# Kernel tuning notes

Hardware: AMD Instinct MI355X
Metric: run time of the kernel (lower is better)

Reference implementation:

```python
import jax, jax.numpy as jnp
import numpy as np

NUM_LABELS = 1024
NUM_CAMS = 8


def setup_inputs() -> dict:
    key = jax.random.key(0)
    k1, k2, k3 = jax.random.split(key, 3)
    feats = jax.random.normal(k1, (16384, 2048), dtype=jnp.float32)
    labels = jax.random.randint(k2, (16384,), 0, NUM_LABELS, dtype=jnp.int64)
    cam_ids = jax.random.randint(k3, (16384,), 0, NUM_CAMS, dtype=jnp.int64)
    return {"feats": feats, "labels": labels, "cam_ids": cam_ids}


def reference(feats, labels, cam_ids):
    # Combined (person-id, camera-id) segment id -> fused segment-mean.
    seg = labels * NUM_CAMS + cam_ids  # [N]
    num_segments = NUM_LABELS * NUM_CAMS
    sums = jax.ops.segment_sum(feats, seg, num_segments=num_segments)  # [S, D]
    counts = jax.ops.segment_sum(jnp.ones_like(seg, dtype=feats.dtype), seg,
                                 num_segments=num_segments)  # [S]
    means = sums / jnp.maximum(counts, 1.0)[:, None]
    # targets[i] = mean of feats over group(label_i, cam_i); detached in torch.
    targets = jax.lax.stop_gradient(means[seg])  # [N, D]
    # SmoothL1 (beta=1), reduction='mean'
    d = feats - targets
    ad = jnp.abs(d)
    loss = jnp.mean(jnp.where(ad < 1.0, 0.5 * d * d, ad - 0.5))
    return loss
```

## Files before the change

### kernel.cpp

```cpp
#include <hip/hip_runtime.h>
#include <hip/hip_bf16.h>

#define N_ROWS 16384
#define D_COLS 2048
#define NUM_LABELS 1024
#define NUM_CAMS 8
#define NUM_SEG (NUM_LABELS * NUM_CAMS)
#define MAXPER 64

__global__ void build_lists_kernel(const int* __restrict__ labels,
                                   const int* __restrict__ cams,
                                   int* __restrict__ counts,
                                   int* __restrict__ lists) {
    int i = blockIdx.x * blockDim.x + threadIdx.x;
    if (i < N_ROWS) {
        int seg = labels[i] * NUM_CAMS + cams[i];
        int pos = atomicAdd(&counts[seg], 1);
        if (pos < MAXPER) lists[seg * MAXPER + pos] = i;
    }
}

__device__ __forceinline__ float smooth_l1(float d) {
    float ad = fabsf(d);
    return ad < 1.0f ? 0.5f * d * d : ad - 0.5f;
}

__global__ __launch_bounds__(256) void seg_loss_kernel(const float* __restrict__ feats,
                                                       const int* __restrict__ counts,
                                                       const int* __restrict__ lists,
                                                       float* __restrict__ partials) {
    int seg = blockIdx.x;
    int tid = threadIdx.x;
    int cnt = counts[seg];
    float local = 0.0f;

    __shared__ int slist[MAXPER];

    if (cnt > 0) {
        int rows = cnt < MAXPER ? cnt : MAXPER;

        if (tid < rows) slist[tid] = lists[seg * MAXPER + tid];
        __syncthreads();

        float m0x = 0.f, m0y = 0.f, m0z = 0.f, m0w = 0.f;
        float m1x = 0.f, m1y = 0.f, m1z = 0.f, m1w = 0.f;

        for (int r = 0; r < rows; ++r) {
            const float4* rp = (const float4*)(feats + (size_t)slist[r] * D_COLS);
            float4 a = rp[tid];
            float4 b = rp[tid + 256];
            m0x += a.x; m0y += a.y; m0z += a.z; m0w += a.w;
            m1x += b.x; m1y += b.y; m1z += b.z; m1w += b.w;
        }
        float inv = 1.0f / (float)cnt;
        m0x *= inv; m0y *= inv; m0z *= inv; m0w *= inv;
        m1x *= inv; m1y *= inv; m1z *= inv; m1w *= inv;

        for (int r = 0; r < rows; ++r) {
            const float4* rp = (const float4*)(feats + (size_t)slist[r] * D_COLS);
            float4 a = rp[tid];
            float4 b = rp[tid + 256];
            local += smooth_l1(a.x - m0x) + smooth_l1(a.y - m0y)
                   + smooth_l1(a.z - m0z) + smooth_l1(a.w - m0w);
            local += smooth_l1(b.x - m1x) + smooth_l1(b.y - m1y)
                   + smooth_l1(b.z - m1z) + smooth_l1(b.w - m1w);
        }
    }

    for (int o = 32; o > 0; o >>= 1)
        local += __shfl_down(local, o, 64);

    __shared__ float wsum[4];
    int lane = tid & 63;
    int wid  = tid >> 6;
    if (lane == 0) wsum[wid] = local;
    __syncthreads();
    if (tid == 0)
        partials[seg] = wsum[0] + wsum[1] + wsum[2] + wsum[3];
}

__global__ __launch_bounds__(256) void reduce_kernel(const float* __restrict__ partials,
                                                     float* __restrict__ out) {
    int tid = threadIdx.x;
    float s = 0.0f;
    for (int i = tid; i < NUM_SEG; i += 256)
        s += partials[i];

    for (int o = 32; o > 0; o >>= 1)
        s += __shfl_down(s, o, 64);

    __shared__ float wsum[4];
    int lane = tid & 63;
    int wid  = tid >> 6;
    if (lane == 0) wsum[wid] = s;
    __syncthreads();
    if (tid == 0)
        out[0] = (wsum[0] + wsum[1] + wsum[2] + wsum[3])
               * (1.0f / ((float)N_ROWS * (float)D_COLS));
}

extern "C" void kernel_launch(void* const* d_in, const int* in_sizes, int n_in,
                              void* d_out, int out_size, void* d_ws, size_t ws_size,
                              hipStream_t stream) {
    const float* feats = (const float*)d_in[0];
    const int* labels  = (const int*)d_in[1];
    const int* cams    = (const int*)d_in[2];
    float* out = (float*)d_out;

    int* counts     = (int*)d_ws;
    int* lists      = counts + NUM_SEG;
    float* partials = (float*)(lists + NUM_SEG * MAXPER);

    hipMemsetAsync(counts, 0, NUM_SEG * sizeof(int), stream);

    build_lists_kernel<<<(N_ROWS + 255) / 256, 256, 0, stream>>>(labels, cams, counts, lists);
    seg_loss_kernel<<<NUM_SEG, 256, 0, stream>>>(feats, counts, lists, partials);
    reduce_kernel<<<1, 256, 0, stream>>>(partials, out);
}
```

Baseline: 213.6 us.

## Assign each half-segment to one wavefront, drop shared memory and block syncs

Reworks the segment loss kernel so each 64-lane wavefront handles half the columns of one segment, with 4 float4 loads per row per lane instead of 2. Row indices are held in lane registers and broadcast with __shfl, which removes the shared-memory list and __syncthreads barriers. Each wave writes its own partial, so the final reduce now covers twice as many partials. The intent is finer-grained scheduling and more loads in flight per thread, at the cost of more accumulator registers and the row-index load being repeated by both waves of a segment.

Result: slower. 219.0 us (+2.6%).

```diff
diff --git a/kernel.cpp b/kernel.cpp
--- a/kernel.cpp
+++ b/kernel.cpp
@@ -7,6 +7,8 @@
 #define NUM_CAMS 8
 #define NUM_SEG (NUM_LABELS * NUM_CAMS)
 #define MAXPER 64
+#define F4_PER_ROW (D_COLS / 4)
+#define NUM_WAVES (NUM_SEG * 2)
 
 __global__ void build_lists_kernel(const int* __restrict__ labels,
                                    const int* __restrict__ cams,
@@ -29,61 +31,73 @@
                                                        const int* __restrict__ counts,
                                                        const int* __restrict__ lists,
                                                        float* __restrict__ partials) {
-    int seg = blockIdx.x;
-    int tid = threadIdx.x;
-    int cnt = counts[seg];
-    float local = 0.0f;
-
-    __shared__ int slist[MAXPER];
+    int wave = (blockIdx.x * 256 + threadIdx.x) >> 6;
+    int lane = threadIdx.x & 63;
+    int seg  = wave >> 1;
+    int half = wave & 1;
+    int cnt  = counts[seg];
+    float loss = 0.0f;
 
     if (cnt > 0) {
         int rows = cnt < MAXPER ? cnt : MAXPER;
 
-        if (tid < rows) slist[tid] = lists[seg * MAXPER + tid];
-        __syncthreads();
+        int myidx = (lane < rows) ? lists[seg * MAXPER + lane] : 0;
 
-        float m0x = 0.f, m0y = 0.f, m0z = 0.f, m0w = 0.f;
-        float m1x = 0.f, m1y = 0.f, m1z = 0.f, m1w = 0.f;
+        const float4* base = (const float4*)feats;
+        int coff = half * 256 + lane;
+
+        float s0x=0.f,s0y=0.f,s0z=0.f,s0w=0.f;
+        float s1x=0.f,s1y=0.f,s1z=0.f,s1w=0.f;
+        float s2x=0.f,s2y=0.f,s2z=0.f,s2w=0.f;
+        float s3x=0.f,s3y=0.f,s3z=0.f,s3w=0.f;
 
         for (int r = 0; r < rows; ++r) {
-            const float4* rp = (const float4*)(feats + (size_t)slist[r] * D_COLS);
-            float4 a = rp[tid];
-            float4 b = rp[tid + 256];
-            m0x += a.x; m0y += a.y; m0z += a.z; m0w += a.w;
-            m1x += b.x; m1y += b.y; m1z += b.z; m1w += b.w;
+            int row = __shfl(myidx, r, 64);
+            const float4* rp = base + (size_t)row * F4_PER_ROW + coff;
+            float4 t0 = rp[0];
+            float4 t1 = rp[64];
+            float4 t2 = rp[128];
+            float4 t3 = rp[192];
+            s0x += t0.x; s0y += t0.y; s0z += t0.z; s0w += t0.w;
+            s1x += t1.x; s1y += t1.y; s1z += t1.z; s1w += t1.w;
+            s2x += t2.x; s2y += t2.y; s2z += t2.z; s2w += t2.w;
+            s3x += t3.x; s3y += t3.y; s3z += t3.z; s3w += t3.w;
         }
         float inv = 1.0f / (float)cnt;
-        m0x *= inv; m0y *= inv; m0z *= inv; m0w *= inv;
-        m1x *= inv; m1y *= inv; m1z *= inv; m1w *= inv;
+        s0x*=inv; s0y*=inv; s0z*=inv; s0w*=inv;
+        s1x*=inv; s1y*=inv; s1z*=inv; s1w*=inv;
+        s2x*=inv; s2y*=inv; s2z*=inv; s2w*=inv;
+        s3x*=inv; s3y*=inv; s3z*=inv; s3w*=inv;
 
         for (int r = 0; r < rows; ++r) {
-            const float4* rp = (const float4*)(feats + (size_t)slist[r] * D_COLS);
-            float4 a = rp[tid];
-            float4 b = rp[tid + 256];
-            local += smooth_l1(a.x - m0x) + smooth_l1(a.y - m0y)
-                   + smooth_l1(a.z - m0z) + smooth_l1(a.w - m0w);
-            local += smooth_l1(b.x - m1x) + smooth_l1(b.y - m1y)
-                   + smooth_l1(b.z - m1z) + smooth_l1(b.w - m1w);
+            int row = __shfl(myidx, r, 64);
+            const float4* rp = base + (size_t)row * F4_PER_ROW + coff;
+            float4 t0 = rp[0];
+            float4 t1 = rp[64];
+            float4 t2 = rp[128];
+            float4 t3 = rp[192];
+            loss += smooth_l1(t0.x - s0x) + smooth_l1(t0.y - s0y)
+                  + smooth_l1(t0.z - s0z) + smooth_l1(t0.w - s0w);
+            loss += smooth_l1(t1.x - s1x) + smooth_l1(t1.y - s1y)
+                  + smooth_l1(t1.z - s1z) + smooth_l1(t1.w - s1w);
+            loss += smooth_l1(t2.x - s2x) + smooth_l1(t2.y - s2y)
+                  + smooth_l1(t2.z - s2z) + smooth_l1(t2.w - s2w);
+            loss += smooth_l1(t3.x - s3x) + smooth_l1(t3.y - s3y)
+                  + smooth_l1(t3.z - s3z) + smooth_l1(t3.w - s3w);
         }
     }
 
     for (int o = 32; o > 0; o >>= 1)
-        local += __shfl_down(local, o, 64);
-
-    __shared__ float wsum[4];
-    int lane = tid & 63;
-    int wid  = tid >> 6;
-    if (lane == 0) wsum[wid] = local;
-    __syncthreads();
-    if (tid == 0)
-        partials[seg] = wsum[0] + wsum[1] + wsum[2] + wsum[3];
+        loss += __shfl_down(loss, o, 64);
+    if (lane == 0)
+        partials[wave] = loss;
 }
 
 __global__ __launch_bounds__(256) void reduce_kernel(const float* __restrict__ partials,
                                                      float* __restrict__ out) {
     int tid = threadIdx.x;
     float s = 0.0f;
-    for (int i = tid; i < NUM_SEG; i += 256)
+    for (int i = tid; i < NUM_WAVES; i += 256)
         s += partials[i];
 
     for (int o = 32; o > 0; o >>= 1)
@@ -114,6 +128,6 @@
     hipMemsetAsync(counts, 0, NUM_SEG * sizeof(int), stream);
 
     build_lists_kernel<<<(N_ROWS + 255) / 256, 256, 0, stream>>>(labels, cams, counts, lists);
-    seg_loss_kernel<<<NUM_SEG, 256, 0, stream>>>(feats, counts, lists, partials);
+    seg_loss_kernel<<<NUM_WAVES * 64 / 256, 256, 0, stream>>>(feats, counts, lists, partials);
     reduce_kernel<<<1, 256, 0, stream>>>(partials, out);
 }
```

## Cache segment rows in registers and split each segment across two blocks

Applied to the files above, without the earlier changes.

Each segment is now handled by two blocks, each covering half of the columns, which doubles the grid and gives each thread one float4 per row instead of two. Up to 12 rows per segment are loaded once into registers and reused for both the mean pass and the loss pass, which removes the second global read for typical segment sizes (about 2 rows on average). Loads are issued unconditionally, using masked list indices and zero weights, so they can all be in flight at once. The cost is extra loads for unused slots (stale list entries, masked into range) and higher register pressure.

New measurement: 224.3 us. 1.05x slower.

```diff
diff --git a/kernel.cpp b/kernel.cpp
--- a/kernel.cpp
+++ b/kernel.cpp
@@ -7,6 +7,9 @@
 #define NUM_CAMS 8
 #define NUM_SEG (NUM_LABELS * NUM_CAMS)
 #define MAXPER 64
+#define R_REG 12
+#define F4_PER_ROW (D_COLS / 4)
+#define NUM_BLOCKS (NUM_SEG * 2)
 
 __global__ void build_lists_kernel(const int* __restrict__ labels,
                                    const int* __restrict__ cams,
@@ -29,61 +32,76 @@
                                                        const int* __restrict__ counts,
                                                        const int* __restrict__ lists,
                                                        float* __restrict__ partials) {
-    int seg = blockIdx.x;
-    int tid = threadIdx.x;
+    int bid  = blockIdx.x;
+    int seg  = bid >> 1;
+    int half = bid & 1;
+    int tid  = threadIdx.x;
+
+    __shared__ int slist[R_REG];
+
+    if (tid < R_REG)
+        slist[tid] = lists[seg * MAXPER + tid] & (N_ROWS - 1);
     int cnt = counts[seg];
-    float local = 0.0f;
+    __syncthreads();
 
-    __shared__ int slist[MAXPER];
+    int rows = cnt < MAXPER ? cnt : MAXPER;
 
-    if (cnt > 0) {
-        int rows = cnt < MAXPER ? cnt : MAXPER;
+    const float4* base = (const float4*)feats + (half * 256 + tid);
 
-        if (tid < rows) slist[tid] = lists[seg * MAXPER + tid];
-        __syncthreads();
+    float4 v[R_REG];
+#pragma unroll
+    for (int r = 0; r < R_REG; ++r)
+        v[r] = base[(size_t)slist[r] * F4_PER_ROW];
 
-        float m0x = 0.f, m0y = 0.f, m0z = 0.f, m0w = 0.f;
-        float m1x = 0.f, m1y = 0.f, m1z = 0.f, m1w = 0.f;
+    float mx = 0.f, my = 0.f, mz = 0.f, mw = 0.f;
+#pragma unroll
+    for (int r = 0; r < R_REG; ++r) {
+        float w = (r < rows) ? 1.0f : 0.0f;
+        mx = fmaf(w, v[r].x, mx);
+        my = fmaf(w, v[r].y, my);
+        mz = fmaf(w, v[r].z, mz);
+        mw = fmaf(w, v[r].w, mw);
+    }
+    for (int r = R_REG; r < rows; ++r) {
+        int row = lists[seg * MAXPER + r];
+        float4 a = base[(size_t)row * F4_PER_ROW];
+        mx += a.x; my += a.y; mz += a.z; mw += a.w;
+    }
 
-        for (int r = 0; r < rows; ++r) {
-            const float4* rp = (const float4*)(feats + (size_t)slist[r] * D_COLS);
-            float4 a = rp[tid];
-            float4 b = rp[tid + 256];
-            m0x += a.x; m0y += a.y; m0z += a.z; m0w += a.w;
-            m1x += b.x; m1y += b.y; m1z += b.z; m1w += b.w;
-        }
-        float inv = 1.0f / (float)cnt;
-        m0x *= inv; m0y *= inv; m0z *= inv; m0w *= inv;
-        m1x *= inv; m1y *= inv; m1z *= inv; m1w *= inv;
+    float inv = 1.0f / (float)(cnt > 0 ? cnt : 1);
+    mx *= inv; my *= inv; mz *= inv; mw *= inv;
 
-        for (int r = 0; r < rows; ++r) {
-            const float4* rp = (const float4*)(feats + (size_t)slist[r] * D_COLS);
-            float4 a = rp[tid];
-            float4 b = rp[tid + 256];
-            local += smooth_l1(a.x - m0x) + smooth_l1(a.y - m0y)
-                   + smooth_l1(a.z - m0z) + smooth_l1(a.w - m0w);
-            local += smooth_l1(b.x - m1x) + smooth_l1(b.y - m1y)
-                   + smooth_l1(b.z - m1z) + smooth_l1(b.w - m1w);
-        }
+    float loss = 0.0f;
+#pragma unroll
+    for (int r = 0; r < R_REG; ++r) {
+        float w = (r < rows) ? 1.0f : 0.0f;
+        loss += w * (smooth_l1(v[r].x - mx) + smooth_l1(v[r].y - my)
+                   + smooth_l1(v[r].z - mz) + smooth_l1(v[r].w - mw));
+    }
+    for (int r = R_REG; r < rows; ++r) {
+        int row = lists[seg * MAXPER + r];
+        float4 a = base[(size_t)row * F4_PER_ROW];
+        loss += smooth_l1(a.x - mx) + smooth_l1(a.y - my)
+              + smooth_l1(a.z - mz) + smooth_l1(a.w - mw);
     }
 
     for (int o = 32; o > 0; o >>= 1)
-        local += __shfl_down(local, o, 64);
+        loss += __shfl_down(loss, o, 64);
 
     __shared__ float wsum[4];
     int lane = tid & 63;
     int wid  = tid >> 6;
-    if (lane == 0) wsum[wid] = local;
+    if (lane == 0) wsum[wid] = loss;
     __syncthreads();
     if (tid == 0)
-        partials[seg] = wsum[0] + wsum[1] + wsum[2] + wsum[3];
+        partials[bid] = wsum[0] + wsum[1] + wsum[2] + wsum[3];
 }
 
 __global__ __launch_bounds__(256) void reduce_kernel(const float* __restrict__ partials,
                                                      float* __restrict__ out) {
     int tid = threadIdx.x;
     float s = 0.0f;
-    for (int i = tid; i < NUM_SEG; i += 256)
+    for (int i = tid; i < NUM_BLOCKS; i += 256)
         s += partials[i];
 
     for (int o = 32; o > 0; o >>= 1)
@@ -114,6 +132,6 @@
     hipMemsetAsync(counts, 0, NUM_SEG * sizeof(int), stream);
 
     build_lists_kernel<<<(N_ROWS + 255) / 256, 256, 0, stream>>>(labels, cams, counts, lists);
-    seg_loss_kernel<<<NUM_SEG, 256, 0, stream>>>(feats, counts, lists, partials);
+    seg_loss_kernel<<<NUM_BLOCKS, 256, 0, stream>>>(feats, counts, lists, partials);
     reduce_kernel<<<1, 256, 0, stream>>>(partials, out);
 }
```
